# Performance work log

Measured on AMD Instinct MI355X. Metric: run time of the kernel, lower is better.

The kernel has to match this reference:

```python
import jax, jax.numpy as jnp
import numpy as np

B, T, C = 2, 1024, 1024
NH, HS, BD, HORIZON = 16, 64, 16, 64


def setup_inputs() -> dict:
    key = jax.random.key(0)
    ks = jax.random.split(key, 16)
    s = 0.02
    return {
        "x": jax.random.normal(ks[0], (B, T, C), jnp.float32),
        "W_disp": jax.random.normal(ks[1], (NH * BD, C), jnp.float32) * s,
        "b_disp": jnp.zeros((NH * BD,), jnp.float32),
        "W_val": jax.random.normal(ks[2], (C, C), jnp.float32) * s,
        "b_val": jnp.zeros((C,), jnp.float32),
        "rel_pos_emb": jax.random.normal(ks[3], (HORIZON, BD), jnp.float32) * s,
        "W_fused": jax.random.normal(ks[4], (2 * BD, BD), jnp.float32) * s,
        "b_fused": jnp.zeros((2 * BD,), jnp.float32),
        "W_pos": jax.random.normal(ks[5], (BD, BD), jnp.float32) * s,
        "W_bond": jax.random.normal(ks[6], (BD,), jnp.float32) * s,
        "b_bond": jnp.zeros((), jnp.float32),
        "W_dmg": jax.random.normal(ks[7], (BD,), jnp.float32) * s,
        "b_dmg": jnp.full((), -3.0, jnp.float32),  # nn.init.constant_(damage_out.bias, -3.0)
        "W_cproj": jax.random.normal(ks[8], (C, C), jnp.float32) * s,
        "b_cproj": jnp.zeros((C,), jnp.float32),
    }


def reference(x, W_disp, b_disp, W_val, b_val, rel_pos_emb, W_fused, b_fused,
              W_pos, W_bond, b_bond, W_dmg, b_dmg, W_cproj, b_cproj):
    delta = min(HORIZON, T)
    gelu = lambda z: jax.nn.gelu(z, approximate=False)  # torch F.gelu default (erf)

    # projections + head split: (B,nh,T,bd) / (B,nh,T,hs)
    disp = (x @ W_disp.T + b_disp).reshape(B, T, NH, BD).transpose(0, 2, 1, 3)
    val = (x @ W_val.T + b_val).reshape(B, T, NH, HS).transpose(0, 2, 1, 3)

    pad = delta - 1
    disp_pad = jnp.pad(disp, ((0, 0), (0, 0), (pad, 0), (0, 0)))
    idx = jnp.arange(T)[:, None] + jnp.arange(delta)[None, :]  # (T,delta) into padded axis
    disp_win = disp_pad[:, :, idx]                      # (B,nh,T,delta,bd)
    strain = disp_win - disp[:, :, :, None, :]          # bond strain

    fused = strain @ W_fused.T + b_fused                # (B,nh,T,delta,2bd)
    bond_f, dmg_f = fused[..., :BD], fused[..., BD:]
    pos_feat = rel_pos_emb[:delta] @ W_pos.T            # (delta,bd)

    bond_logits = gelu(bond_f + pos_feat) @ W_bond + b_bond          # (B,nh,T,delta)
    damage = jax.nn.sigmoid(gelu(dmg_f) @ W_dmg + b_dmg)             # (B,nh,T,delta)
    logits = bond_logits - 10.0 * damage

    cmask = (jnp.arange(T)[:, None] - delta + 1 + jnp.arange(delta)[None, :]) >= 0
    logits = jnp.where(cmask[None, None], logits, -jnp.inf)
    weights = jax.nn.softmax(logits, axis=-1)           # (B,nh,T,delta)

    # weighted sum over window without materializing (B,nh,T,delta,hs)
    val_pad = jnp.pad(val, ((0, 0), (0, 0), (pad, 0), (0, 0)))
    def body(acc, j):
        sl = jax.lax.dynamic_slice_in_dim(val_pad, j, T, axis=2)  # (B,nh,T,hs)
        return acc + weights[..., j][..., None] * sl, None
    out0 = jnp.zeros((B, NH, T, HS), jnp.float32)
    out, _ = jax.lax.scan(body, out0, jnp.arange(delta))

    y = out.transpose(0, 2, 1, 3).reshape(B, T, C)
    return y @ W_cproj.T + b_cproj
```

## Files before the change

kernel.cpp:

```cpp
#include <hip/hip_runtime.h>

#define BDIM 16
#define HSZ 64
#define NHEAD 16
#define DELTA 64
#define LOG2E 1.4426950408889634f

typedef __bf16 bf16x8 __attribute__((ext_vector_type(8)));
typedef float f32x4 __attribute__((ext_vector_type(4)));
typedef float f32x2 __attribute__((ext_vector_type(2)));
typedef unsigned short us8 __attribute__((ext_vector_type(8)));
typedef unsigned int u32;

__device__ __forceinline__ unsigned short f2bf(float f) {
    u32 u = __float_as_uint(f);
    return (unsigned short)((u + 0x7fffu + ((u >> 16) & 1u)) >> 16);
}
__device__ __forceinline__ float bf2f(unsigned short s) {
    return __uint_as_float(((u32)s) << 16);
}

__device__ __forceinline__ void gload_lds16(const void* g, void* l) {
    __builtin_amdgcn_global_load_lds(
        (const __attribute__((address_space(1))) void*)g,
        (__attribute__((address_space(3))) void*)l, 16, 0, 0);
}

__global__ __launch_bounds__(256) void cast4_bf16(
    const float* __restrict__ s0, unsigned short* __restrict__ d0,
    const float* __restrict__ s1, unsigned short* __restrict__ d1,
    const float* __restrict__ s2, unsigned short* __restrict__ d2,
    const float* __restrict__ s3, unsigned short* __restrict__ d3,
    const float* __restrict__ bd, const float* __restrict__ bv,
    float* __restrict__ bcat) {
    int blk = blockIdx.x;
    if (blk == 4352) {
        for (int t = threadIdx.x; t < 320; t += 256) {
            if (t < 64) ((float4*)bcat)[t] = ((const float4*)bd)[t];
            else        ((float4*)bcat)[t] = ((const float4*)bv)[t - 64];
        }
        return;
    }
    const float* src; unsigned short* dst; int base;
    if (blk < 2048)      { src = s0; dst = d0; base = blk; }
    else if (blk < 2304) { src = s1; dst = d1; base = blk - 2048; }
    else if (blk < 3328) { src = s2; dst = d2; base = blk - 2304; }
    else                 { src = s3; dst = d3; base = blk - 3328; }
    int i = base * 256 + threadIdx.x;
    float4 f = ((const float4*)src)[i];
    ushort4 o;
    o.x = f2bf(f.x); o.y = f2bf(f.y); o.z = f2bf(f.z); o.w = f2bf(f.w);
    ((ushort4*)dst)[i] = o;
}

__global__ __launch_bounds__(256) void gemm_bf16(const unsigned short* __restrict__ A,
                                                 const unsigned short* __restrict__ Bw,
                                                 const float* __restrict__ bias,
                                                 float* __restrict__ C,
                                                 unsigned short* __restrict__ CbT,
                                                 int N, int K, int nbx, int mode) {
    __shared__ __align__(16) unsigned short lA[2][8 * 512];
    __shared__ __align__(16) unsigned short lB[2][8 * 512];
    int tid = threadIdx.x;
    int w = tid >> 6, lane = tid & 63;
    int id = blockIdx.x;
    int xcd = id & 7, rr = id >> 3;
    int mi = xcd * 4 + (rr & 3);
    int ni = rr >> 2;
    int bm = mi * 64, bn = ni * 64;
    int wr = w & 1, wc = w >> 1;
    int m16 = lane & 15, q = lane >> 4;

    const unsigned short* aPtr[2];
    const unsigned short* bPtr[2];
#pragma unroll
    for (int i = 0; i < 2; ++i) {
        int g = w + 4 * i;
        aPtr[i] = A + (long)(bm + (g & 3) * 16 + m16) * K + (g >> 2) * 32 + q * 8;
        bPtr[i] = Bw + (long)(bn + (g & 3) * 16 + m16) * K + (g >> 2) * 32 + q * 8;
    }

    f32x4 acc[2][2];
#pragma unroll
    for (int i = 0; i < 2; ++i)
#pragma unroll
        for (int j = 0; j < 2; ++j) acc[i][j] = (f32x4){0.f, 0.f, 0.f, 0.f};

    int nk = K >> 6;
#pragma unroll
    for (int i = 0; i < 2; ++i) {
        gload_lds16(aPtr[i], &lA[0][(w + 4 * i) * 512]);
        gload_lds16(bPtr[i], &lB[0][(w + 4 * i) * 512]);
    }

    for (int kt = 0; kt < nk; ++kt) {
        int p = kt & 1;
        __syncthreads();
        if (kt + 1 < nk) {
            int ko = (kt + 1) * 64;
#pragma unroll
            for (int i = 0; i < 2; ++i) {
                gload_lds16(aPtr[i] + ko, &lA[p ^ 1][(w + 4 * i) * 512]);
                gload_lds16(bPtr[i] + ko, &lB[p ^ 1][(w + 4 * i) * 512]);
            }
        }
#pragma unroll
        for (int s = 0; s < 2; ++s) {
            bf16x8 af[2], bg[2];
#pragma unroll
            for (int r = 0; r < 2; ++r) {
                af[r] = *(const bf16x8*)&lA[p][(s * 4 + wr * 2 + r) * 512 + lane * 8];
                bg[r] = *(const bf16x8*)&lB[p][(s * 4 + wc * 2 + r) * 512 + lane * 8];
            }
#pragma unroll
            for (int r = 0; r < 2; ++r)
#pragma unroll
                for (int n = 0; n < 2; ++n)
                    acc[r][n] = __builtin_amdgcn_mfma_f32_16x16x32_bf16(af[r], bg[n], acc[r][n], 0, 0, 0);
        }
    }

    if (mode == 0 || bn < 256) {
        int ldc = (mode == 0) ? N : 256;
#pragma unroll
        for (int n = 0; n < 2; ++n) {
            int col = bn + wc * 32 + n * 16 + m16;
            float bv = bias[col];
#pragma unroll
            for (int r = 0; r < 2; ++r)
#pragma unroll
                for (int e = 0; e < 4; ++e) {
                    int row = bm + wr * 32 + r * 16 + q * 4 + e;
                    C[(long)row * ldc + col] = acc[r][n][e] + bv;
                }
        }
    } else {
        __syncthreads();
        unsigned short* sC = (unsigned short*)&lA[0][0];
#pragma unroll
        for (int n = 0; n < 2; ++n) {
            int col_l = wc * 32 + n * 16 + m16;
            float bv = bias[bn + col_l];
#pragma unroll
            for (int r = 0; r < 2; ++r)
#pragma unroll
                for (int e = 0; e < 4; ++e) {
                    int row_l = wr * 32 + r * 16 + q * 4 + e;
                    sC[row_l * 64 + col_l] = f2bf(acc[r][n][e] + bv);
                }
        }
        __syncthreads();
        long base0 = ((long)(bm >> 10)) * 1048576 + (long)(bn - 256) * 1024 + (bm & 1023);
#pragma unroll
        for (int it = 0; it < 2; ++it) {
            int slot = it * 256 + tid;
            int hs = slot >> 3;
            int tc = (slot & 7) * 8;
            us8 o;
#pragma unroll
            for (int j = 0; j < 8; ++j) o[j] = sC[(tc + j) * 64 + hs];
            *(us8*)&CbT[base0 + (long)hs * 1024 + tc] = o;
        }
    }
}

__device__ __forceinline__ f32x2 gelu2(f32x2 z) {
    f32x2 z2 = z * z;
    f32x2 u = z * (0.7978845608f + 0.0356774081f * z2);
    f32x2 u2 = u * u;
    f32x2 den = 1.f + 0.33333333f * u2;
    f32x2 r;
    r.x = __builtin_amdgcn_rcpf(den.x);
    r.y = __builtin_amdgcn_rcpf(den.y);
    f32x2 th = u * r;
    f32x2 zh = 0.5f * z;
    return zh + zh * th;
}

#define PROJ_LD 36
#define VW_LD 136

__global__ __launch_bounds__(512) void attn_kernel(
    const float* __restrict__ disp,
    const unsigned short* __restrict__ valT,
    const float* __restrict__ rel,
    const float* __restrict__ Wpos,
    const float* __restrict__ Wf,
    const float* __restrict__ bfu,
    const float* __restrict__ Wb,
    const float* __restrict__ bb_p,
    const float* __restrict__ Wd,
    const float* __restrict__ bd_p,
    unsigned short* __restrict__ y,
    int T) {
    __shared__ __align__(16) unsigned short sWd[64 * VW_LD];
    __shared__ __align__(16) float ov[128 * PROJ_LD + 128 * 16 + 512];
    float* sProj = ov;
    float* sDisp = ov + 128 * PROJ_LD;
    float* sWfT  = sDisp + 128 * 16;
    unsigned short* sValT = (unsigned short*)ov;

    int tid = threadIdx.x;
    int ntile = T / 64;
    int t0 = (blockIdx.x % ntile) * 64;
    int bh = blockIdx.x / ntile;
    int b = bh / NHEAD, h = bh % NHEAD;
    int wave = tid >> 6, lane = tid & 63;
    int m16 = lane & 15, q = lane >> 4;

    {
        uint4 z4 = make_uint4(0, 0, 0, 0);
        for (int i = tid; i < 1088; i += 512) ((uint4*)sWd)[i] = z4;
        sWfT[(tid & 15) * 32 + (tid >> 4)] = Wf[tid];
        {
            int r = tid >> 2, qq = tid & 3;
            int ts = t0 + r - 64;
            float4 v = make_float4(0.f, 0.f, 0.f, 0.f);
            if (ts >= 0)
                v = ((const float4*)(disp + ((long)(b * T + ts) * NHEAD + h) * BDIM))[qq];
            *(float4*)&sDisp[r * 16 + qq * 4] = v;
        }
    }
    __syncthreads();
    for (int idx = tid; idx < 128 * 32; idx += 512) {
        int r = idx >> 5, k = idx & 31;
        float a = 0.f;
#pragma unroll
        for (int d = 0; d < 16; ++d) a += sDisp[r * 16 + d] * sWfT[d * 32 + k];
        sProj[r * PROJ_LD + k] = a;
    }

    float relv[16];
#pragma unroll
    for (int e = 0; e < 4; ++e) {
        float4 rr = ((const float4*)rel)[lane * 4 + e];
        relv[e * 4 + 0] = rr.x; relv[e * 4 + 1] = rr.y;
        relv[e * 4 + 2] = rr.z; relv[e * 4 + 3] = rr.w;
    }
    f32x2 pfd[16], wbd[16];
#pragma unroll
    for (int d = 0; d < 16; ++d) {
        float a = 0.f;
#pragma unroll
        for (int e = 0; e < 16; ++e) a += relv[e] * Wpos[d * 16 + e];
        pfd[d].x = a + bfu[d];
        pfd[d].y = bfu[16 + d];
        wbd[d].x = Wb[d];
        wbd[d].y = Wd[d];
    }
    float bbond = *bb_p, bdmg = *bd_p;
    __syncthreads();

    int wbase = wave * 8;
    for (int rr = 0; rr < 8; ++rr) {
        int tl = wbase + rr;
        int rs = tl + 1 + lane;
        int rc = tl + 64;
        bool valid = (t0 + tl + lane - 63) >= 0;
        float cb[16], cd[16], pb[16], pd[16];
        const float* crow = &sProj[rc * PROJ_LD];
        const float* prow = &sProj[rs * PROJ_LD];
#pragma unroll
        for (int qq = 0; qq < 4; ++qq) {
            float4 v1 = *(const float4*)&crow[qq * 4];
            float4 v2 = *(const float4*)&crow[16 + qq * 4];
            float4 v3 = *(const float4*)&prow[qq * 4];
            float4 v4 = *(const float4*)&prow[16 + qq * 4];
            cb[qq*4+0]=v1.x; cb[qq*4+1]=v1.y; cb[qq*4+2]=v1.z; cb[qq*4+3]=v1.w;
            cd[qq*4+0]=v2.x; cd[qq*4+1]=v2.y; cd[qq*4+2]=v2.z; cd[qq*4+3]=v2.w;
            pb[qq*4+0]=v3.x; pb[qq*4+1]=v3.y; pb[qq*4+2]=v3.z; pb[qq*4+3]=v3.w;
            pd[qq*4+0]=v4.x; pd[qq*4+1]=v4.y; pd[qq*4+2]=v4.z; pd[qq*4+3]=v4.w;
        }
        f32x2 acc2 = (f32x2){bbond, bdmg};
#pragma unroll
        for (int k = 0; k < 16; ++k) {
            f32x2 pz, cz;
            pz.x = pb[k]; pz.y = pd[k];
            cz.x = cb[k]; cz.y = cd[k];
            f32x2 z = pz - cz + pfd[k];
            acc2 = acc2 + gelu2(z) * wbd[k];
        }
        float bl = acc2.x, dm = acc2.y;
        float damage = __builtin_amdgcn_rcpf(1.f + __builtin_exp2f(-dm * LOG2E));
        float logit = bl - 10.f * damage;
        float e = valid ? __builtin_exp2f(logit * LOG2E) : 0.f;
        float ssum = e;
#pragma unroll
        for (int off = 32; off >= 1; off >>= 1) ssum += __shfl_xor(ssum, off);
        sWd[tl * VW_LD + rs] = f2bf(e * __builtin_amdgcn_rcpf(ssum));
    }
    __syncthreads();

    {
        int hs = lane;
        long vbase = ((long)(b * NHEAD * HSZ + h * HSZ + hs)) * T + (t0 - 64);
#pragma unroll
        for (int it = 0; it < 2; ++it) {
            int g = wave * 2 + it;
            int ts0 = t0 - 64 + g * 8;
            us8 v = (us8)0;
            if (ts0 >= 0) v = *(const us8*)&valT[vbase + g * 8];
            *(us8*)&sValT[hs * VW_LD + g * 8] = v;
        }
    }
    __syncthreads();

    {
        int mi = wave >> 1;
        int nh = (wave & 1) * 2;
        int kt0 = mi >> 1;
        f32x4 acc[2];
#pragma unroll
        for (int n = 0; n < 2; ++n) acc[n] = (f32x4){0.f, 0.f, 0.f, 0.f};
#pragma unroll
        for (int kk = 0; kk < 3; ++kk) {
            int kt = kt0 + kk;
            bf16x8 a = *(const bf16x8*)&sWd[(mi * 16 + m16) * VW_LD + kt * 32 + q * 8];
#pragma unroll
            for (int n = 0; n < 2; ++n) {
                bf16x8 bv = *(const bf16x8*)&sValT[((nh + n) * 16 + m16) * VW_LD + kt * 32 + q * 8];
                acc[n] = __builtin_amdgcn_mfma_f32_16x16x32_bf16(a, bv, acc[n], 0, 0, 0);
            }
        }
        int trow = t0 + mi * 16 + q * 4;
#pragma unroll
        for (int n = 0; n < 2; ++n) {
            int col = h * HSZ + (nh + n) * 16 + m16;
#pragma unroll
            for (int e = 0; e < 4; ++e)
                y[(long)(b * T + trow + e) * (NHEAD * HSZ) + col] = f2bf(acc[n][e]);
        }
    }
}

extern "C" void kernel_launch(void* const* d_in, const int* in_sizes, int n_in,
                              void* d_out, int out_size, void* d_ws, size_t ws_size,
                              hipStream_t stream) {
    const float* x       = (const float*)d_in[0];
    const float* W_disp  = (const float*)d_in[1];
    const float* b_disp  = (const float*)d_in[2];
    const float* W_val   = (const float*)d_in[3];
    const float* b_val   = (const float*)d_in[4];
    const float* rel     = (const float*)d_in[5];
    const float* W_fused = (const float*)d_in[6];
    const float* b_fused = (const float*)d_in[7];
    const float* W_pos   = (const float*)d_in[8];
    const float* W_bond  = (const float*)d_in[9];
    const float* b_bond  = (const float*)d_in[10];
    const float* W_dmg   = (const float*)d_in[11];
    const float* b_dmg   = (const float*)d_in[12];
    const float* W_cproj = (const float*)d_in[13];
    const float* b_cproj = (const float*)d_in[14];
    float* out = (float*)d_out;
    float* ws  = (float*)d_ws;

    const int B = 2, T = 1024, C = 1024;
    float* disp = ws;
    float* bcat = disp + 524288;
    unsigned short* x_bf  = (unsigned short*)(bcat + 1280);
    unsigned short* valT  = x_bf + 2097152;
    unsigned short* Wcat  = valT + 2097152;
    unsigned short* Wv_bf = Wcat + 262144;
    unsigned short* Wc_bf = Wv_bf + 1048576;
    unsigned short* y_bf  = x_bf;

    cast4_bf16<<<4353, 256, 0, stream>>>(x, x_bf, W_disp, Wcat, W_val, Wv_bf,
                                         W_cproj, Wc_bf, b_disp, b_val, bcat);

    gemm_bf16<<<640, 256, 0, stream>>>(x_bf, Wcat, bcat, disp, valT,
                                       1280, C, 20, 1);
    attn_kernel<<<dim3(B * NHEAD * (T / 64)), 512, 0, stream>>>(
        disp, valT, rel, W_pos, W_fused, b_fused, W_bond, b_bond, W_dmg, b_dmg,
        y_bf, T);
    gemm_bf16<<<512, 256, 0, stream>>>(y_bf, Wc_bf, b_cproj, out, nullptr,
                                       C, C, 16, 0);
}
```

Baseline: 166.4 us.

## Fuse all stages into one persistent kernel with atomic grid barriers

Replaces the four launches (cast, QKV GEMM, attention, output GEMM) with a single persistent kernel of 256 blocks of 512 threads, separated by atomic-counter grid barriers. GEMM tiles grow to 128x64 with 8 waves, and each block handles several attention tiles. The aim is to remove launch overhead and the gaps between kernels. In exchange it adds barrier spin cost, possible load imbalance (only 64 blocks take a second GEMM tile), and a memset launch, and it depends on all 256 blocks being co-resident.

```diff
diff --git a/kernel.cpp b/kernel.cpp
--- a/kernel.cpp
+++ b/kernel.cpp
@@ -3,7 +3,6 @@
 #define BDIM 16
 #define HSZ 64
 #define NHEAD 16
-#define DELTA 64
 #define LOG2E 1.4426950408889634f
 
 typedef __bf16 bf16x8 __attribute__((ext_vector_type(8)));
@@ -16,9 +15,6 @@
     u32 u = __float_as_uint(f);
     return (unsigned short)((u + 0x7fffu + ((u >> 16) & 1u)) >> 16);
 }
-__device__ __forceinline__ float bf2f(unsigned short s) {
-    return __uint_as_float(((u32)s) << 16);
-}
 
 __device__ __forceinline__ void gload_lds16(const void* g, void* l) {
     __builtin_amdgcn_global_load_lds(
@@ -26,92 +22,64 @@
         (__attribute__((address_space(3))) void*)l, 16, 0, 0);
 }
 
-__global__ __launch_bounds__(256) void cast4_bf16(
-    const float* __restrict__ s0, unsigned short* __restrict__ d0,
-    const float* __restrict__ s1, unsigned short* __restrict__ d1,
-    const float* __restrict__ s2, unsigned short* __restrict__ d2,
-    const float* __restrict__ s3, unsigned short* __restrict__ d3,
-    const float* __restrict__ bd, const float* __restrict__ bv,
-    float* __restrict__ bcat) {
-    int blk = blockIdx.x;
-    if (blk == 4352) {
-        for (int t = threadIdx.x; t < 320; t += 256) {
-            if (t < 64) ((float4*)bcat)[t] = ((const float4*)bd)[t];
-            else        ((float4*)bcat)[t] = ((const float4*)bv)[t - 64];
-        }
-        return;
-    }
-    const float* src; unsigned short* dst; int base;
-    if (blk < 2048)      { src = s0; dst = d0; base = blk; }
-    else if (blk < 2304) { src = s1; dst = d1; base = blk - 2048; }
-    else if (blk < 3328) { src = s2; dst = d2; base = blk - 2304; }
-    else                 { src = s3; dst = d3; base = blk - 3328; }
-    int i = base * 256 + threadIdx.x;
-    float4 f = ((const float4*)src)[i];
-    ushort4 o;
-    o.x = f2bf(f.x); o.y = f2bf(f.y); o.z = f2bf(f.z); o.w = f2bf(f.w);
-    ((ushort4*)dst)[i] = o;
-}
-
-__global__ __launch_bounds__(256) void gemm_bf16(const unsigned short* __restrict__ A,
-                                                 const unsigned short* __restrict__ Bw,
-                                                 const float* __restrict__ bias,
-                                                 float* __restrict__ C,
-                                                 unsigned short* __restrict__ CbT,
-                                                 int N, int K, int nbx, int mode) {
-    __shared__ __align__(16) unsigned short lA[2][8 * 512];
-    __shared__ __align__(16) unsigned short lB[2][8 * 512];
-    int tid = threadIdx.x;
+__device__ __forceinline__ void gsync(unsigned* bar, unsigned target) {
+    __syncthreads();
+    if (threadIdx.x == 0) {
+        __hip_atomic_fetch_add(bar, 1u, __ATOMIC_ACQ_REL, __HIP_MEMORY_SCOPE_AGENT);
+        while (__hip_atomic_load(bar, __ATOMIC_ACQUIRE, __HIP_MEMORY_SCOPE_AGENT) < target) {
+            __builtin_amdgcn_s_sleep(8);
+        }
+    }
+    __syncthreads();
+}
+
+__device__ __forceinline__ void gemm_tile(
+    unsigned char* smem, const unsigned short* __restrict__ A,
+    const unsigned short* __restrict__ Bw, const float* __restrict__ bias,
+    float* __restrict__ C, unsigned short* __restrict__ CbT,
+    int N, int K, int bm, int bn, int mode, int tid) {
+    unsigned short* lA = (unsigned short*)smem;
+    unsigned short* lB = (unsigned short*)(smem + 32768);
     int w = tid >> 6, lane = tid & 63;
-    int id = blockIdx.x;
-    int xcd = id & 7, rr = id >> 3;
-    int mi = xcd * 4 + (rr & 3);
-    int ni = rr >> 2;
-    int bm = mi * 64, bn = ni * 64;
-    int wr = w & 1, wc = w >> 1;
+    int wr = w & 3, wc = w >> 2;
     int m16 = lane & 15, q = lane >> 4;
 
-    const unsigned short* aPtr[2];
-    const unsigned short* bPtr[2];
-#pragma unroll
-    for (int i = 0; i < 2; ++i) {
-        int g = w + 4 * i;
-        aPtr[i] = A + (long)(bm + (g & 3) * 16 + m16) * K + (g >> 2) * 32 + q * 8;
-        bPtr[i] = Bw + (long)(bn + (g & 3) * 16 + m16) * K + (g >> 2) * 32 + q * 8;
-    }
+    __syncthreads();
+
+    int ga0 = w, ga1 = w + 8;
+    const unsigned short* aPtr0 = A + (long)(bm + (ga0 & 7) * 16 + m16) * K + (ga0 >> 3) * 32 + q * 8;
+    const unsigned short* aPtr1 = A + (long)(bm + (ga1 & 7) * 16 + m16) * K + (ga1 >> 3) * 32 + q * 8;
+    const unsigned short* bPtr  = Bw + (long)(bn + (w & 3) * 16 + m16) * K + (w >> 2) * 32 + q * 8;
 
     f32x4 acc[2][2];
 #pragma unroll
-    for (int i = 0; i < 2; ++i)
-#pragma unroll
-        for (int j = 0; j < 2; ++j) acc[i][j] = (f32x4){0.f, 0.f, 0.f, 0.f};
+    for (int r = 0; r < 2; ++r)
+#pragma unroll
+        for (int n = 0; n < 2; ++n) acc[r][n] = (f32x4){0.f, 0.f, 0.f, 0.f};
 
     int nk = K >> 6;
-#pragma unroll
-    for (int i = 0; i < 2; ++i) {
-        gload_lds16(aPtr[i], &lA[0][(w + 4 * i) * 512]);
-        gload_lds16(bPtr[i], &lB[0][(w + 4 * i) * 512]);
-    }
+    gload_lds16(aPtr0, &lA[ga0 * 512]);
+    gload_lds16(aPtr1, &lA[ga1 * 512]);
+    gload_lds16(bPtr, &lB[w * 512]);
 
     for (int kt = 0; kt < nk; ++kt) {
         int p = kt & 1;
         __syncthreads();
         if (kt + 1 < nk) {
             int ko = (kt + 1) * 64;
-#pragma unroll
-            for (int i = 0; i < 2; ++i) {
-                gload_lds16(aPtr[i] + ko, &lA[p ^ 1][(w + 4 * i) * 512]);
-                gload_lds16(bPtr[i] + ko, &lB[p ^ 1][(w + 4 * i) * 512]);
-            }
+            gload_lds16(aPtr0 + ko, &lA[(p ^ 1) * 8192 + ga0 * 512]);
+            gload_lds16(aPtr1 + ko, &lA[(p ^ 1) * 8192 + ga1 * 512]);
+            gload_lds16(bPtr + ko, &lB[(p ^ 1) * 4096 + w * 512]);
         }
 #pragma unroll
         for (int s = 0; s < 2; ++s) {
             bf16x8 af[2], bg[2];
 #pragma unroll
-            for (int r = 0; r < 2; ++r) {
-                af[r] = *(const bf16x8*)&lA[p][(s * 4 + wr * 2 + r) * 512 + lane * 8];
-                bg[r] = *(const bf16x8*)&lB[p][(s * 4 + wc * 2 + r) * 512 + lane * 8];
-            }
+            for (int r = 0; r < 2; ++r)
+                af[r] = *(const bf16x8*)&lA[p * 8192 + (s * 8 + wr * 2 + r) * 512 + lane * 8];
+#pragma unroll
+            for (int n = 0; n < 2; ++n)
+                bg[n] = *(const bf16x8*)&lB[p * 4096 + (s * 4 + wc * 2 + n) * 512 + lane * 8];
 #pragma unroll
             for (int r = 0; r < 2; ++r)
 #pragma unroll
@@ -136,7 +104,7 @@
         }
     } else {
         __syncthreads();
-        unsigned short* sC = (unsigned short*)&lA[0][0];
+        unsigned short* sC = lA;
 #pragma unroll
         for (int n = 0; n < 2; ++n) {
             int col_l = wc * 32 + n * 16 + m16;
@@ -153,9 +121,9 @@
         long base0 = ((long)(bm >> 10)) * 1048576 + (long)(bn - 256) * 1024 + (bm & 1023);
 #pragma unroll
         for (int it = 0; it < 2; ++it) {
-            int slot = it * 256 + tid;
-            int hs = slot >> 3;
-            int tc = (slot & 7) * 8;
+            int slot = it * 512 + tid;
+            int hs = slot >> 4;
+            int tc = (slot & 15) * 8;
             us8 o;
 #pragma unroll
             for (int j = 0; j < 8; ++j) o[j] = sC[(tc + j) * 64 + hs];
@@ -180,33 +148,29 @@
 #define PROJ_LD 36
 #define VW_LD 136
 
-__global__ __launch_bounds__(512) void attn_kernel(
-    const float* __restrict__ disp,
-    const unsigned short* __restrict__ valT,
-    const float* __restrict__ rel,
-    const float* __restrict__ Wpos,
-    const float* __restrict__ Wf,
-    const float* __restrict__ bfu,
-    const float* __restrict__ Wb,
-    const float* __restrict__ bb_p,
-    const float* __restrict__ Wd,
-    const float* __restrict__ bd_p,
-    unsigned short* __restrict__ y,
-    int T) {
-    __shared__ __align__(16) unsigned short sWd[64 * VW_LD];
-    __shared__ __align__(16) float ov[128 * PROJ_LD + 128 * 16 + 512];
+__device__ __forceinline__ void attn_tile(
+    unsigned char* smem, const float* __restrict__ disp,
+    const unsigned short* __restrict__ valT, const float* __restrict__ rel,
+    const float* __restrict__ Wpos, const float* __restrict__ Wf,
+    const float* __restrict__ bfu, const float* __restrict__ Wb,
+    const float* __restrict__ bb_p, const float* __restrict__ Wd,
+    const float* __restrict__ bd_p, unsigned short* __restrict__ y,
+    int tile, int tid) {
+    const int T = 1024;
+    unsigned short* sWd = (unsigned short*)smem;
+    float* ov = (float*)(smem + 17408);
     float* sProj = ov;
     float* sDisp = ov + 128 * PROJ_LD;
     float* sWfT  = sDisp + 128 * 16;
     unsigned short* sValT = (unsigned short*)ov;
 
-    int tid = threadIdx.x;
-    int ntile = T / 64;
-    int t0 = (blockIdx.x % ntile) * 64;
-    int bh = blockIdx.x / ntile;
-    int b = bh / NHEAD, h = bh % NHEAD;
+    int t0 = (tile & 15) * 64;
+    int bh = tile >> 4;
+    int b = bh >> 4, h = bh & 15;
     int wave = tid >> 6, lane = tid & 63;
     int m16 = lane & 15, q = lane >> 4;
+
+    __syncthreads();
 
     {
         uint4 z4 = make_uint4(0, 0, 0, 0);
@@ -330,6 +294,69 @@
             for (int e = 0; e < 4; ++e)
                 y[(long)(b * T + trow + e) * (NHEAD * HSZ) + col] = f2bf(acc[n][e]);
         }
+    }
+}
+
+__global__ __launch_bounds__(512, 2) void fused_all(
+    const float* __restrict__ x, const float* __restrict__ Wd_w,
+    const float* __restrict__ bdp, const float* __restrict__ Wv_w,
+    const float* __restrict__ bvp, const float* __restrict__ rel,
+    const float* __restrict__ Wf, const float* __restrict__ bfu,
+    const float* __restrict__ Wpos, const float* __restrict__ Wb,
+    const float* __restrict__ bb_p, const float* __restrict__ Wdm,
+    const float* __restrict__ bd_p, const float* __restrict__ Wc_w,
+    const float* __restrict__ bc, float* __restrict__ out,
+    float* __restrict__ disp, float* __restrict__ bcat,
+    unsigned short* __restrict__ x_bf, unsigned short* __restrict__ valT,
+    unsigned short* __restrict__ Wcat, unsigned short* __restrict__ Wv_bf,
+    unsigned short* __restrict__ Wc_bf, unsigned short* __restrict__ y_bf,
+    unsigned* bar) {
+    __shared__ __align__(16) unsigned char smem[49152];
+    int tid = threadIdx.x;
+    int bid = blockIdx.x;
+
+    {
+        int gid = bid * 512 + tid;
+        for (int i = gid; i < 1114112; i += 131072) {
+            const float* src; unsigned short* dst; int j;
+            if (i < 524288)      { src = x;    dst = x_bf;  j = i; }
+            else if (i < 589824) { src = Wd_w; dst = Wcat;  j = i - 524288; }
+            else if (i < 851968) { src = Wv_w; dst = Wv_bf; j = i - 589824; }
+            else                 { src = Wc_w; dst = Wc_bf; j = i - 851968; }
+            float4 f = ((const float4*)src)[j];
+            ushort4 o;
+            o.x = f2bf(f.x); o.y = f2bf(f.y); o.z = f2bf(f.z); o.w = f2bf(f.w);
+            ((ushort4*)dst)[j] = o;
+        }
+        if (bid == 255 && tid < 320) {
+            if (tid < 64) ((float4*)bcat)[tid] = ((const float4*)bdp)[tid];
+            else          ((float4*)bcat)[tid] = ((const float4*)bvp)[tid - 64];
+        }
+    }
+    gsync(bar, 256);
+
+    {
+        int mi = bid & 15, ni = bid >> 4;
+        gemm_tile(smem, x_bf, Wcat, bcat, disp, valT, 1280, 1024,
+                  mi * 128, ni * 64, 1, tid);
+        if (bid < 64) {
+            int t2 = 256 + bid;
+            gemm_tile(smem, x_bf, Wcat, bcat, disp, valT, 1280, 1024,
+                      (t2 & 15) * 128, (t2 >> 4) * 64, 1, tid);
+        }
+    }
+    gsync(bar, 512);
+
+    attn_tile(smem, disp, valT, rel, Wpos, Wf, bfu, Wb, bb_p, Wdm, bd_p,
+              y_bf, bid, tid);
+    attn_tile(smem, disp, valT, rel, Wpos, Wf, bfu, Wb, bb_p, Wdm, bd_p,
+              y_bf, bid + 256, tid);
+    gsync(bar, 768);
+
+    {
+        int mi = bid & 15, ni = bid >> 4;
+        gemm_tile(smem, y_bf, Wc_bf, bc, out, nullptr, 1024, 1024,
+                  mi * 128, ni * 64, 0, tid);
     }
 }
 
@@ -354,7 +381,6 @@
     float* out = (float*)d_out;
     float* ws  = (float*)d_ws;
 
-    const int B = 2, T = 1024, C = 1024;
     float* disp = ws;
     float* bcat = disp + 524288;
     unsigned short* x_bf  = (unsigned short*)(bcat + 1280);
@@ -363,15 +389,12 @@
     unsigned short* Wv_bf = Wcat + 262144;
     unsigned short* Wc_bf = Wv_bf + 1048576;
     unsigned short* y_bf  = x_bf;
-
-    cast4_bf16<<<4353, 256, 0, stream>>>(x, x_bf, W_disp, Wcat, W_val, Wv_bf,
-                                         W_cproj, Wc_bf, b_disp, b_val, bcat);
-
-    gemm_bf16<<<640, 256, 0, stream>>>(x_bf, Wcat, bcat, disp, valT,
-                                       1280, C, 20, 1);
-    attn_kernel<<<dim3(B * NHEAD * (T / 64)), 512, 0, stream>>>(
-        disp, valT, rel, W_pos, W_fused, b_fused, W_bond, b_bond, W_dmg, b_dmg,
-        y_bf, T);
-    gemm_bf16<<<512, 256, 0, stream>>>(y_bf, Wc_bf, b_cproj, out, nullptr,
-                                       C, C, 16, 0);
-}
+    unsigned* bar = (unsigned*)((char*)d_ws + (32u << 20));
+
+    hipMemsetAsync(bar, 0, 256, stream);
+
+    fused_all<<<256, 512, 0, stream>>>(
+        x, W_disp, b_disp, W_val, b_val, rel, W_fused, b_fused, W_pos,
+        W_bond, b_bond, W_dmg, b_dmg, W_cproj, b_cproj, out,
+        disp, bcat, x_bf, valT, Wcat, Wv_bf, Wc_bf, y_bf, bar);
+}
```

After: 253.3 us. 52.3% more time.

## Triple-buffer GEMM LDS loads with explicit vmcnt waits and barriers

Applied to the files above, without the earlier changes.

Replaces the double-buffered global-to-LDS pipeline in the bf16 GEMM with a three-stage ring buffer. Two tiles are prefetched ahead, and completion is tracked with manual s_waitcnt vmcnt counts, raw s_barrier and sched_barrier fences. The aim is to hide more global-load latency behind the MFMA work. In exchange it uses more LDS per block, which can lower occupancy, and correctness depends on the hand-computed vmcnt values matching the number of outstanding loads.

```diff
diff --git a/kernel.cpp b/kernel.cpp
--- a/kernel.cpp
+++ b/kernel.cpp
@@ -59,8 +59,8 @@
                                                  float* __restrict__ C,
                                                  unsigned short* __restrict__ CbT,
                                                  int N, int K, int nbx, int mode) {
-    __shared__ __align__(16) unsigned short lA[2][8 * 512];
-    __shared__ __align__(16) unsigned short lB[2][8 * 512];
+    __shared__ __align__(16) unsigned short lA[3][8 * 512];
+    __shared__ __align__(16) unsigned short lB[3][8 * 512];
     int tid = threadIdx.x;
     int w = tid >> 6, lane = tid & 63;
     int id = blockIdx.x;
@@ -87,38 +87,57 @@
         for (int j = 0; j < 2; ++j) acc[i][j] = (f32x4){0.f, 0.f, 0.f, 0.f};
 
     int nk = K >> 6;
-#pragma unroll
-    for (int i = 0; i < 2; ++i) {
-        gload_lds16(aPtr[i], &lA[0][(w + 4 * i) * 512]);
-        gload_lds16(bPtr[i], &lB[0][(w + 4 * i) * 512]);
-    }
-
-    for (int kt = 0; kt < nk; ++kt) {
-        int p = kt & 1;
-        __syncthreads();
-        if (kt + 1 < nk) {
-            int ko = (kt + 1) * 64;
-#pragma unroll
-            for (int i = 0; i < 2; ++i) {
-                gload_lds16(aPtr[i] + ko, &lA[p ^ 1][(w + 4 * i) * 512]);
-                gload_lds16(bPtr[i] + ko, &lB[p ^ 1][(w + 4 * i) * 512]);
-            }
-        }
-#pragma unroll
-        for (int s = 0; s < 2; ++s) {
-            bf16x8 af[2], bg[2];
-#pragma unroll
-            for (int r = 0; r < 2; ++r) {
-                af[r] = *(const bf16x8*)&lA[p][(s * 4 + wr * 2 + r) * 512 + lane * 8];
-                bg[r] = *(const bf16x8*)&lB[p][(s * 4 + wc * 2 + r) * 512 + lane * 8];
-            }
-#pragma unroll
-            for (int r = 0; r < 2; ++r)
-#pragma unroll
-                for (int n = 0; n < 2; ++n)
-                    acc[r][n] = __builtin_amdgcn_mfma_f32_16x16x32_bf16(af[r], bg[n], acc[r][n], 0, 0, 0);
-        }
-    }
+
+#define ISSUE_STEP(KT, BUF)                                                 \
+    {                                                                       \
+        int ko = (KT) * 64;                                                 \
+        _Pragma("unroll")                                                   \
+        for (int i = 0; i < 2; ++i) {                                       \
+            gload_lds16(aPtr[i] + ko, &lA[BUF][(w + 4 * i) * 512]);         \
+            gload_lds16(bPtr[i] + ko, &lB[BUF][(w + 4 * i) * 512]);         \
+        }                                                                   \
+    }
+#define MFMA_STEP(CUR)                                                      \
+    {                                                                       \
+        _Pragma("unroll")                                                   \
+        for (int s = 0; s < 2; ++s) {                                       \
+            bf16x8 af[2], bg[2];                                            \
+            _Pragma("unroll")                                               \
+            for (int r = 0; r < 2; ++r) {                                   \
+                af[r] = *(const bf16x8*)&lA[CUR][(s * 4 + wr * 2 + r) * 512 + lane * 8]; \
+                bg[r] = *(const bf16x8*)&lB[CUR][(s * 4 + wc * 2 + r) * 512 + lane * 8]; \
+            }                                                               \
+            _Pragma("unroll")                                               \
+            for (int r = 0; r < 2; ++r)                                     \
+                _Pragma("unroll")                                           \
+                for (int n = 0; n < 2; ++n)                                 \
+                    acc[r][n] = __builtin_amdgcn_mfma_f32_16x16x32_bf16(af[r], bg[n], acc[r][n], 0, 0, 0); \
+        }                                                                   \
+    }
+
+    ISSUE_STEP(0, 0);
+    ISSUE_STEP(1, 1);
+    ISSUE_STEP(2, 2);
+
+    int cur = 0;
+    for (int kt = 0; kt < nk - 2; ++kt) {
+        asm volatile("s_waitcnt vmcnt(8)\n\ts_barrier" ::: "memory");
+        __builtin_amdgcn_sched_barrier(0);
+        MFMA_STEP(cur);
+        __builtin_amdgcn_sched_barrier(0);
+        asm volatile("s_barrier" ::: "memory");
+        if (kt + 3 < nk) ISSUE_STEP(kt + 3, cur);
+        cur = (cur == 2) ? 0 : cur + 1;
+    }
+    asm volatile("s_waitcnt vmcnt(4)\n\ts_barrier" ::: "memory");
+    __builtin_amdgcn_sched_barrier(0);
+    MFMA_STEP(cur);
+    cur = (cur == 2) ? 0 : cur + 1;
+    asm volatile("s_waitcnt vmcnt(0)\n\ts_barrier" ::: "memory");
+    __builtin_amdgcn_sched_barrier(0);
+    MFMA_STEP(cur);
+#undef ISSUE_STEP
+#undef MFMA_STEP
 
     if (mode == 0 || bn < 256) {
         int ldc = (mode == 0) ? N : 256;
```

New measurement: 165.6 us. Within noise of the previous version (-0.4%).
